# Optimization experiments

Measured on AMD Instinct MI355X. Metric: run time of the kernel, lower is better.

Reference implementation:

```python
import jax, jax.numpy as jnp
import numpy as np

D_MODEL = 1024
N_HEADS = 16
HEAD_DIM = D_MODEL // N_HEADS
ROPE_THETA = 10000.0


def _apply_rope(t, pos):
    # t: [B, H, S, hd]; pos: [B, S] int. Half-split (NeoX-style) rotation.
    hd = t.shape[-1]
    inv_freq = 1.0 / (ROPE_THETA ** (jnp.arange(0, hd, 2, dtype=t.dtype) / hd))  # [hd/2]
    ang = pos.astype(t.dtype)[:, None, :, None] * inv_freq  # [B, 1, S, hd/2]
    cos, sin = jnp.cos(ang), jnp.sin(ang)
    t1, t2 = t[..., 0::2], t[..., 1::2]
    r1 = t1 * cos - t2 * sin
    r2 = t1 * sin + t2 * cos
    # interleave back
    return jnp.stack([r1, r2], axis=-1).reshape(t.shape)


def setup_inputs() -> dict:
    key = jax.random.key(0)
    k1, k2, k3 = jax.random.split(key, 3)
    B, S = 4, 2048
    x = jax.random.normal(k1, (B, S, D_MODEL), dtype=jnp.float32)
    positions = jnp.broadcast_to(jnp.arange(S, dtype=jnp.int32), (B, S))
    Wqkv = jax.random.normal(k2, (3 * D_MODEL, D_MODEL), dtype=jnp.float32) * (1.0 / np.sqrt(D_MODEL))
    bqkv = jnp.zeros((3 * D_MODEL,), dtype=jnp.float32)
    Wo = jax.random.normal(k3, (D_MODEL, D_MODEL), dtype=jnp.float32) * (1.0 / np.sqrt(D_MODEL))
    bo = jnp.zeros((D_MODEL,), dtype=jnp.float32)
    return {"x": x, "positions": positions, "Wqkv": Wqkv, "bqkv": bqkv, "Wo": Wo, "bo": bo}


def reference(x, positions, Wqkv, bqkv, Wo, bo):
    B, S, D = x.shape
    # fused QKV projection (torch Linear: x @ W^T + b)
    qkv = x @ Wqkv.T + bqkv                      # [B, S, 3D]
    q, k, v = jnp.split(qkv, 3, axis=-1)
    def to_heads(t):
        return t.reshape(B, S, N_HEADS, HEAD_DIM).transpose(0, 2, 1, 3)  # [B, H, S, hd]
    q, k, v = to_heads(q), to_heads(k), to_heads(v)
    q = _apply_rope(q, positions)
    k = _apply_rope(k, positions)
    scale = 1.0 / np.sqrt(HEAD_DIM)
    scores = jnp.einsum('bhqd,bhkd->bhqk', q, k) * scale   # [B, H, S, S]
    causal = jnp.tril(jnp.ones((S, S), dtype=bool))
    scores = jnp.where(causal, scores, jnp.finfo(scores.dtype).min)
    attn = jax.nn.softmax(scores, axis=-1)
    h = jnp.einsum('bhqk,bhkd->bhqd', attn, v)             # [B, H, S, hd]
    h = h.transpose(0, 2, 1, 3).reshape(B, S, D)
    return h @ Wo.T + bo
```

## Files before the change

### kernel.cpp

```cpp
#include <hip/hip_runtime.h>

#define DEV static __device__ __forceinline__

typedef __attribute__((ext_vector_type(8))) short short8;
typedef __attribute__((ext_vector_type(4))) short short4v;
typedef __attribute__((ext_vector_type(4))) float f32x4;
typedef __attribute__((ext_vector_type(4))) unsigned short ushort4v;
typedef __attribute__((ext_vector_type(4))) float float4v;

#define DM 1024
#define NH 16
#define HD 64
#define SS 2048
#define TOK 8192

DEV unsigned short f2bf(float f) {
  union { float f; unsigned u; } v; v.f = f;
  unsigned r = v.u + 0x7FFFu + ((v.u >> 16) & 1u);
  return (unsigned short)(r >> 16);
}
DEV float bf2f(unsigned short h) {
  union { unsigned u; float f; } v; v.u = ((unsigned)h) << 16;
  return v.f;
}

#define MFMA16x32(a, b, c) __builtin_amdgcn_mfma_f32_16x16x32_bf16((a), (b), (c), 0, 0, 0)

DEV f32x4 mfma_pv(short4v a, short4v b, f32x4 c) {
#if __has_builtin(__builtin_amdgcn_mfma_f32_16x16x16bf16_1k)
  return __builtin_amdgcn_mfma_f32_16x16x16bf16_1k(a, b, c, 0, 0, 0);
#else
  f32x4 d;
  asm("v_mfma_f32_16x16x16_bf16 %0, %1, %2, %3" : "=&v"(d) : "v"(a), "v"(b), "v"(c));
  return d;
#endif
}

DEV void gload_lds16(const unsigned short* g, unsigned short* l) {
  __builtin_amdgcn_global_load_lds(
      (const __attribute__((address_space(1))) void*)g,
      (__attribute__((address_space(3))) void*)l, 16, 0, 0);
}

__global__ __launch_bounds__(256) void k_prep(const float* __restrict__ x,
                                              unsigned short* __restrict__ x_bf,
                                              const float* __restrict__ Wqkv,
                                              unsigned short* __restrict__ wqkv_bf,
                                              const float* __restrict__ Wo,
                                              unsigned short* __restrict__ wo_bf,
                                              const int* __restrict__ pos,
                                              float* __restrict__ tc,
                                              float* __restrict__ ts) {
  int blk = blockIdx.x;
  if (blk < 8192) {
    int i = blk * 256 + threadIdx.x;
    float4v v = ((const float4v*)x)[i];
    ushort4v o;
    o[0] = f2bf(v[0]); o[1] = f2bf(v[1]); o[2] = f2bf(v[2]); o[3] = f2bf(v[3]);
    ((ushort4v*)x_bf)[i] = o;
  } else if (blk < 11264) {
    int i = (blk - 8192) * 256 + threadIdx.x;
    float4v v = ((const float4v*)Wqkv)[i];
    ushort4v o;
    o[0] = f2bf(v[0]); o[1] = f2bf(v[1]); o[2] = f2bf(v[2]); o[3] = f2bf(v[3]);
    ((ushort4v*)wqkv_bf)[i] = o;
  } else if (blk < 12288) {
    int i = (blk - 11264) * 256 + threadIdx.x;
    float4v v = ((const float4v*)Wo)[i];
    ushort4v o;
    o[0] = f2bf(v[0]); o[1] = f2bf(v[1]); o[2] = f2bf(v[2]); o[3] = f2bf(v[3]);
    ((ushort4v*)wo_bf)[i] = o;
  } else {
    int i = (blk - 12288) * 256 + threadIdx.x;
    int t = i >> 5, fi = i & 31;
    float p = (float)pos[t];
    float inv = powf(10000.0f, -(float)fi / 32.0f);
    float a = p * inv;
    float sv, cv;
    sincosf(a, &sv, &cv);
    tc[i] = cv;
    ts[i] = sv;
  }
}

template <int MODE>
__global__ __launch_bounds__(512) void k_gemm3(
    const unsigned short* __restrict__ A, const unsigned short* __restrict__ Bm,
    const float* __restrict__ bias, void* __restrict__ out0, void* __restrict__ out1,
    void* __restrict__ out2, const float* __restrict__ tabc,
    const float* __restrict__ tabs, int M, int N, int K) {
  __shared__ __align__(16) unsigned short Abuf[3][256 * 64];
  __shared__ __align__(16) unsigned short Bbuf[3][128 * 64];
  const int tid = threadIdx.x;
  const int wid = tid >> 6, lane = tid & 63;
  const int l16 = lane & 15, lq = lane >> 4;
  const int wr = wid >> 1, wc = wid & 1;
  const int r8 = lane >> 3, c8 = lane & 7;
  const int NT = K >> 6;
  const int sx = l16 & 7;

  const int gx = N >> 7;
  const int nwg = gx * (M >> 8);
  const int chunk = nwg >> 3;
  const int bid = blockIdx.x;
  const int virt = (bid & 7) * chunk + (bid >> 3);
  const int m0 = (virt / gx) << 8;
  const int n0 = (virt % gx) << 7;

#define STAGE_G3(T, BSEL)                                                           \
  {                                                                                 \
    int k0_ = (T) << 6;                                                             \
    unsigned short* ab_ = Abuf[BSEL];                                               \
    unsigned short* bb_ = Bbuf[BSEL];                                               \
    _Pragma("unroll")                                                               \
    for (int i_ = 0; i_ < 4; ++i_) {                                                \
      int c_ = wid * 4 + i_;                                                        \
      gload_lds16(A + (size_t)(m0 + c_ * 8 + r8) * K + k0_ + ((c8 ^ r8) << 3),      \
                  &ab_[c_ * 512]);                                                  \
    }                                                                               \
    _Pragma("unroll")                                                               \
    for (int i_ = 0; i_ < 2; ++i_) {                                                \
      int c_ = wid * 2 + i_;                                                        \
      gload_lds16(Bm + (size_t)(n0 + c_ * 8 + r8) * K + k0_ + ((c8 ^ r8) << 3),     \
                  &bb_[c_ * 512]);                                                  \
    }                                                                               \
  }

  f32x4 acc[4][4];
#pragma unroll
  for (int i = 0; i < 4; i++)
#pragma unroll
    for (int j = 0; j < 4; j++) acc[i][j] = (f32x4){0.f, 0.f, 0.f, 0.f};

  STAGE_G3(0, 0)
  STAGE_G3(1, 1)
  asm volatile("s_waitcnt vmcnt(6)" ::: "memory");
  __builtin_amdgcn_s_barrier();
  __builtin_amdgcn_sched_barrier(0);

  int cb = 0, sb = 2;
  for (int t = 0; t < NT; ++t) {
    if (t + 2 < NT) STAGE_G3(t + 2, sb)
    const unsigned short* Ab = Abuf[cb];
    const unsigned short* Bb = Bbuf[cb];
#pragma unroll
    for (int kk = 0; kk < 2; ++kk) {
      int sw0 = ((kk * 4 + lq) ^ sx) << 3;
      short8 af[4], bfr[4];
#pragma unroll
      for (int mi = 0; mi < 4; ++mi)
        af[mi] = *(const short8*)&Ab[(wr * 64 + mi * 16 + l16) * 64 + sw0];
#pragma unroll
      for (int ni = 0; ni < 4; ++ni)
        bfr[ni] = *(const short8*)&Bb[(wc * 64 + ni * 16 + l16) * 64 + sw0];
#pragma unroll
      for (int mi = 0; mi < 4; ++mi)
#pragma unroll
        for (int ni = 0; ni < 4; ++ni)
          acc[mi][ni] = MFMA16x32(af[mi], bfr[ni], acc[mi][ni]);
    }
    if (t + 1 < NT) {
      if (t + 3 <= NT) {
        asm volatile("s_waitcnt vmcnt(6)" ::: "memory");
      } else {
        asm volatile("s_waitcnt vmcnt(0)" ::: "memory");
      }
      __builtin_amdgcn_s_barrier();
      __builtin_amdgcn_sched_barrier(0);
    }
    cb = (cb == 2) ? 0 : cb + 1;
    sb = (sb == 2) ? 0 : sb + 1;
  }
#undef STAGE_G3

  if (MODE == 0) {
    float* C = (float*)out0;
#pragma unroll
    for (int mi = 0; mi < 4; ++mi) {
      int row = m0 + wr * 64 + mi * 16 + lq * 4;
#pragma unroll
      for (int ni = 0; ni < 4; ++ni) {
        int col = n0 + wc * 64 + ni * 16 + l16;
        float bv = bias[col];
#pragma unroll
        for (int j = 0; j < 4; ++j)
          C[(size_t)(row + j) * N + col] = acc[mi][ni][j] + bv;
      }
    }
  } else {
    unsigned short* Qb = (unsigned short*)out0;
    unsigned short* Kb = (unsigned short*)out1;
    unsigned short* Vt = (unsigned short*)out2;
    int sel0 = n0 >> 10;
#pragma unroll
    for (int mi = 0; mi < 4; ++mi) {
      int row = m0 + wr * 64 + mi * 16 + lq * 4;
#pragma unroll
      for (int ni = 0; ni < 4; ++ni) {
        int col = n0 + wc * 64 + ni * 16 + l16;
        int hh = (col >> 6) & 15;
        int d = col & 63;
        float bv = bias[col];
        if (sel0 < 2) {
          unsigned short* P = sel0 ? Kb : Qb;
          int pfr = d >> 1;
          size_t p = ((size_t)((row >> 11) * NH + hh) * SS + (row & 2047)) * 64 + d;
#pragma unroll
          for (int j = 0; j < 4; ++j) {
            float val = acc[mi][ni][j] + bv;
            float part = __shfl_xor(val, 1, 64);
            int rr = row + j;
            float cv = tabc[((size_t)rr << 5) + pfr];
            float sv = tabs[((size_t)rr << 5) + pfr];
            float outv = (d & 1) ? (part * sv + val * cv)
                                 : (val * cv - part * sv);
            P[p + (size_t)j * 64] = f2bf(outv);
          }
        } else {
          size_t p = ((size_t)((row >> 11) * NH + hh) * 64 + d) * SS + (row & 2047);
          ushort4v o;
#pragma unroll
          for (int j = 0; j < 4; ++j) o[j] = f2bf(acc[mi][ni][j] + bv);
          *(ushort4v*)&Vt[p] = o;
        }
      }
    }
  }
}

__global__ __launch_bounds__(512) void k_attn(const unsigned short* __restrict__ Q,
                                              const unsigned short* __restrict__ K,
                                              const unsigned short* __restrict__ Vt,
                                              unsigned short* __restrict__ H) {
  __shared__ __align__(16) unsigned short Kbuf[2 * 4096];
  __shared__ __align__(16) unsigned short Vbuf[2 * 4096];

  int lin = blockIdx.x;
  int bh = lin & 63;
  int g = 15 - (lin >> 6);
  int b = bh >> 4, h = bh & 15;
  int tid = threadIdx.x;
  int wid = tid >> 6, lane = tid & 63;
  int l16 = lane & 15, lq = lane >> 4;
  int sx = l16 & 7;
  const unsigned short* Qh = Q + (size_t)bh * SS * 64;
  const unsigned short* Kh = K + (size_t)bh * SS * 64;
  const unsigned short* Vh = Vt + (size_t)bh * 64 * SS;

  int qbase = g * 128 + wid * 16;
  int qrow = qbase + l16;
  int ktmax = (qbase + 15) >> 6;
  int ntk = 2 * g + 2;

  short8 aq[2];
  {
    const unsigned short* qp = Qh + (size_t)qrow * 64 + lq * 8;
    aq[0] = *(const short8*)qp;
    aq[1] = *(const short8*)(qp + 32);
  }
  f32x4 o[4];
#pragma unroll
  for (int i = 0; i < 4; ++i) o[i] = (f32x4){0.f, 0.f, 0.f, 0.f};
  float lsum = 0.f;

  {
    int c = tid;
    int row = c >> 3, col = ((c & 7) ^ (row & 7)) << 3;
    gload_lds16(Kh + (size_t)row * 64 + col, &Kbuf[c * 8]);
    gload_lds16(Vh + (size_t)row * SS + col, &Vbuf[c * 8]);
  }
  __syncthreads();

  int cur = 0;
  for (int kt = 0; kt < ntk; ++kt) {
    if (kt + 1 < ntk) {
      int kb1 = (kt + 1) << 6;
      int nb_ = (cur ^ 1) * 4096;
      int c = tid;
      int row = c >> 3, col = ((c & 7) ^ (row & 7)) << 3;
      gload_lds16(Kh + (size_t)(kb1 + row) * 64 + col, &Kbuf[nb_ + c * 8]);
      gload_lds16(Vh + (size_t)row * SS + kb1 + col, &Vbuf[nb_ + c * 8]);
    }
    if (kt <= ktmax) {
      int kb = kt << 6;
      const unsigned short* Kb_ = &Kbuf[cur * 4096];
      const unsigned short* Vb_ = &Vbuf[cur * 4096];

      f32x4 sacc[4];
#pragma unroll
      for (int nb = 0; nb < 4; ++nb) {
        int r = nb * 16 + l16;
        short8 bk0 = *(const short8*)&Kb_[r * 64 + ((lq ^ sx) << 3)];
        short8 bk1 = *(const short8*)&Kb_[r * 64 + (((4 | lq) ^ sx) << 3)];
        f32x4 z = (f32x4){0.f, 0.f, 0.f, 0.f};
        z = MFMA16x32(bk0, aq[0], z);
        z = MFMA16x32(bk1, aq[1], z);
        sacc[nb] = z;
      }
      float sc[4][4];
#pragma unroll
      for (int nb = 0; nb < 4; ++nb)
#pragma unroll
        for (int j = 0; j < 4; ++j) sc[nb][j] = sacc[nb][j] * 0.18033688f;
      if (kt == ktmax) {
#pragma unroll
        for (int nb = 0; nb < 4; ++nb)
#pragma unroll
          for (int j = 0; j < 4; ++j) {
            int key = kb + nb * 16 + lq * 4 + j;
            if (key > qrow) sc[nb][j] = -1e30f;
          }
      }
      short4v pa[4];
#pragma unroll
      for (int nb = 0; nb < 4; ++nb) {
        float pv[4];
#pragma unroll
        for (int j = 0; j < 4; ++j) {
          float e;
          asm("v_exp_f32 %0, %1" : "=v"(e) : "v"(sc[nb][j]));
          lsum += e;
          pv[j] = e;
        }
        union { unsigned u[2]; short4v s4; } pk;
        asm("v_cvt_pk_bf16_f32 %0, %1, %2" : "=v"(pk.u[0]) : "v"(pv[0]), "v"(pv[1]));
        asm("v_cvt_pk_bf16_f32 %0, %1, %2" : "=v"(pk.u[1]) : "v"(pv[2]), "v"(pv[3]));
        pa[nb] = pk.s4;
      }
#pragma unroll
      for (int ni = 0; ni < 4; ++ni) {
        int row = ni * 16 + l16;
        f32x4 acc = o[ni];
#pragma unroll
        for (int nb = 0; nb < 4; ++nb) {
          int ch = (2 * nb + (lq >> 1)) ^ sx;
          short4v bv = *(const short4v*)&Vb_[row * 64 + ch * 8 + ((lq & 1) << 2)];
          acc = mfma_pv(pa[nb], bv, acc);
        }
        o[ni] = acc;
      }
    }
    __syncthreads();
    cur ^= 1;
  }

  float red = lsum;
  red += __shfl_xor(red, 16, 64);
  red += __shfl_xor(red, 32, 64);
  float inv[4];
#pragma unroll
  for (int j = 0; j < 4; ++j) {
    int src = (lane & 48) + ((lane >> 4) & 3) * 4 + j;
    inv[j] = 1.0f / __shfl(red, src, 64);
  }
#pragma unroll
  for (int ni = 0; ni < 4; ++ni) {
    int d = h * 64 + ni * 16 + l16;
#pragma unroll
    for (int j = 0; j < 4; ++j) {
      int s = qbase + lq * 4 + j;
      H[((size_t)(b * SS + s)) * 1024 + d] = f2bf(o[ni][j] * inv[j]);
    }
  }
}

extern "C" void kernel_launch(void* const* d_in, const int* in_sizes, int n_in,
                              void* d_out, int out_size, void* d_ws, size_t ws_size,
                              hipStream_t stream) {
  const float* x    = (const float*)d_in[0];
  const int*   pos  = (const int*)d_in[1];
  const float* Wqkv = (const float*)d_in[2];
  const float* bqkv = (const float*)d_in[3];
  const float* Wo   = (const float*)d_in[4];
  const float* bo   = (const float*)d_in[5];
  float* out = (float*)d_out;

  char* w = (char*)d_ws;
  unsigned short* x_bf    = (unsigned short*)(w + 0);
  unsigned short* h_bf    = x_bf;
  unsigned short* wqkv_bf = (unsigned short*)(w + 16777216);
  unsigned short* wo_bf   = (unsigned short*)(w + 23068672);
  unsigned short* Qb      = (unsigned short*)(w + 25165824);
  unsigned short* Kb      = (unsigned short*)(w + 41943040);
  unsigned short* Vt      = (unsigned short*)(w + 58720256);
  float* tabc             = (float*)(w + 75497472);
  float* tabs             = (float*)(w + 76546048);

  k_prep<<<13312, 256, 0, stream>>>(x, x_bf, Wqkv, wqkv_bf, Wo, wo_bf, pos, tabc, tabs);
  k_gemm3<1><<<768, 512, 0, stream>>>(x_bf, wqkv_bf, bqkv, Qb, Kb, Vt, tabc, tabs, TOK, 3072, DM);
  k_attn<<<1024, 512, 0, stream>>>(Qb, Kb, Vt, h_bf);
  k_gemm3<0><<<256, 512, 0, stream>>>(h_bf, wo_bf, bo, out, nullptr, nullptr, tabc, tabs, TOK, DM, DM);
}
```

Baseline: 183.1 us.

## Triple-buffer K/V tiles in attention with prefetch distance two

The attention kernel moves from a double-buffered to a triple-buffered K/V shared-memory ring. Each iteration now issues the global-to-LDS loads for tile kt+2. At the end of the iteration it waits with a partial s_waitcnt vmcnt plus a raw barrier, instead of a full __syncthreads that drains every outstanding load. The goal is to hide more global-memory latency behind the MFMA work. The cost is 50% more LDS per block, which may reduce how many blocks fit on a CU.

```diff
diff --git a/kernel.cpp b/kernel.cpp
--- a/kernel.cpp
+++ b/kernel.cpp
@@ -232,8 +232,8 @@
                                               const unsigned short* __restrict__ K,
                                               const unsigned short* __restrict__ Vt,
                                               unsigned short* __restrict__ H) {
-  __shared__ __align__(16) unsigned short Kbuf[2 * 4096];
-  __shared__ __align__(16) unsigned short Vbuf[2 * 4096];
+  __shared__ __align__(16) unsigned short Kbuf[3 * 4096];
+  __shared__ __align__(16) unsigned short Vbuf[3 * 4096];
 
   int lin = blockIdx.x;
   int bh = lin & 63;
@@ -252,6 +252,18 @@
   int ktmax = (qbase + 15) >> 6;
   int ntk = 2 * g + 2;
 
+  const int srow = tid >> 3;
+  const int scol = ((tid & 7) ^ (srow & 7)) << 3;
+
+#define STAGE_ATT(T, BSEL)                                                      \
+  {                                                                             \
+    int kb_ = (T) << 6;                                                         \
+    gload_lds16(Kh + (size_t)(kb_ + srow) * 64 + scol,                          \
+                &Kbuf[(BSEL) * 4096 + tid * 8]);                                \
+    gload_lds16(Vh + (size_t)srow * SS + kb_ + scol,                            \
+                &Vbuf[(BSEL) * 4096 + tid * 8]);                                \
+  }
+
   short8 aq[2];
   {
     const unsigned short* qp = Qh + (size_t)qrow * 64 + lq * 8;
@@ -263,28 +275,19 @@
   for (int i = 0; i < 4; ++i) o[i] = (f32x4){0.f, 0.f, 0.f, 0.f};
   float lsum = 0.f;
 
-  {
-    int c = tid;
-    int row = c >> 3, col = ((c & 7) ^ (row & 7)) << 3;
-    gload_lds16(Kh + (size_t)row * 64 + col, &Kbuf[c * 8]);
-    gload_lds16(Vh + (size_t)row * SS + col, &Vbuf[c * 8]);
-  }
-  __syncthreads();
-
-  int cur = 0;
+  STAGE_ATT(0, 0)
+  STAGE_ATT(1, 1)
+  asm volatile("s_waitcnt vmcnt(2)" ::: "memory");
+  __builtin_amdgcn_s_barrier();
+  __builtin_amdgcn_sched_barrier(0);
+
+  int cb = 0, sb = 2;
   for (int kt = 0; kt < ntk; ++kt) {
-    if (kt + 1 < ntk) {
-      int kb1 = (kt + 1) << 6;
-      int nb_ = (cur ^ 1) * 4096;
-      int c = tid;
-      int row = c >> 3, col = ((c & 7) ^ (row & 7)) << 3;
-      gload_lds16(Kh + (size_t)(kb1 + row) * 64 + col, &Kbuf[nb_ + c * 8]);
-      gload_lds16(Vh + (size_t)row * SS + kb1 + col, &Vbuf[nb_ + c * 8]);
-    }
+    if (kt + 2 < ntk) STAGE_ATT(kt + 2, sb)
     if (kt <= ktmax) {
       int kb = kt << 6;
-      const unsigned short* Kb_ = &Kbuf[cur * 4096];
-      const unsigned short* Vb_ = &Vbuf[cur * 4096];
+      const unsigned short* Kb_ = &Kbuf[cb * 4096];
+      const unsigned short* Vb_ = &Vbuf[cb * 4096];
 
       f32x4 sacc[4];
 #pragma unroll
@@ -340,9 +343,19 @@
         o[ni] = acc;
       }
     }
-    __syncthreads();
-    cur ^= 1;
-  }
+    if (kt + 1 < ntk) {
+      if (kt + 2 < ntk) {
+        asm volatile("s_waitcnt vmcnt(2)" ::: "memory");
+      } else {
+        asm volatile("s_waitcnt vmcnt(0)" ::: "memory");
+      }
+      __builtin_amdgcn_s_barrier();
+      __builtin_amdgcn_sched_barrier(0);
+    }
+    cb = (cb == 2) ? 0 : cb + 1;
+    sb = (sb == 2) ? 0 : sb + 1;
+  }
+#undef STAGE_ATT
 
   float red = lsum;
   red += __shfl_xor(red, 16, 64);
```

Result: no change. 182.8 us (median of 2 runs) (-0.2%).
